# Kernel tuning notes

Measured on AMD Instinct MI355X. Metric: run time of the kernel, lower is better.

## Reference

```python
import jax, jax.numpy as jnp
import numpy as np


def setup_inputs() -> dict:
    key = jax.random.key(0)
    k1, k2 = jax.random.split(key)
    x1 = jax.random.normal(k1, (8192, 64), dtype=jnp.float32)
    x2 = jax.random.normal(k2, (8192, 64), dtype=jnp.float32)
    return {"x1": x1, "x2": x2}


def reference(x1, x2):
    # squared Euclidean distance: ||a-b||^2 = ||a||^2 + ||b||^2 - 2 a.b
    sq1 = jnp.sum(x1 * x1, axis=-1, keepdims=True)        # [N, 1]
    sq2 = jnp.sum(x2 * x2, axis=-1, keepdims=True).T      # [1, M]
    cross = jnp.einsum('nd,md->nm', x1, x2)               # [N, M] GEMM
    d2 = sq1 + sq2 - 2.0 * cross
    # clamp tiny negatives from floating-point cancellation (cdist>=0)
    return jnp.maximum(d2, 0.0)
```

## Files before the change

### kernel.cpp

```cpp
#include <hip/hip_runtime.h>


typedef __bf16 bf16x8 __attribute__((ext_vector_type(8)));
typedef float floatx4 __attribute__((ext_vector_type(4)));
typedef unsigned short ushort8 __attribute__((ext_vector_type(8)));

#define TILE 128
#define KD 64
#define LDSS 72

__device__ __forceinline__ unsigned short f2bf(float x) {
    union { float f; unsigned int u; } v; v.f = x;
    return (unsigned short)((v.u + 0x7FFFu + ((v.u >> 16) & 1u)) >> 16);
}

__global__ __launch_bounds__(256) void convert_rows(
        const float* __restrict__ x1,
        const float* __restrict__ x2,
        unsigned short* __restrict__ xb1,
        unsigned short* __restrict__ xb2,
        float* __restrict__ sq1,
        float* __restrict__ sq2,
        int N, int M) {
    const int tid = blockIdx.x * blockDim.x + threadIdx.x;
    if (tid >= N + M) return;
    const int r = (tid < N) ? tid : tid - N;
    const float* src = (tid < N) ? (x1 + (size_t)r * KD) : (x2 + (size_t)r * KD);
    unsigned short* dst = (tid < N) ? (xb1 + (size_t)r * KD) : (xb2 + (size_t)r * KD);
    float nrm = 0.f;
    #pragma unroll
    for (int i = 0; i < 8; ++i) {
        const float4 f0 = ((const float4*)src)[2 * i];
        const float4 f1 = ((const float4*)src)[2 * i + 1];
        nrm = fmaf(f0.x, f0.x, nrm); nrm = fmaf(f0.y, f0.y, nrm);
        nrm = fmaf(f0.z, f0.z, nrm); nrm = fmaf(f0.w, f0.w, nrm);
        nrm = fmaf(f1.x, f1.x, nrm); nrm = fmaf(f1.y, f1.y, nrm);
        nrm = fmaf(f1.z, f1.z, nrm); nrm = fmaf(f1.w, f1.w, nrm);
        ushort8 pk;
        pk[0] = f2bf(f0.x); pk[1] = f2bf(f0.y); pk[2] = f2bf(f0.z); pk[3] = f2bf(f0.w);
        pk[4] = f2bf(f1.x); pk[5] = f2bf(f1.y); pk[6] = f2bf(f1.z); pk[7] = f2bf(f1.w);
        *(ushort8*)&dst[i * 8] = pk;
    }
    if (tid < N) sq1[r] = nrm; else sq2[r] = nrm;
}

__global__ __launch_bounds__(256) void sqeuclid_main(
        const unsigned short* __restrict__ xb1,
        const unsigned short* __restrict__ xb2,
        const float* __restrict__ sq1,
        const float* __restrict__ sq2,
        float* __restrict__ out, int M) {
    const int t = threadIdx.x;
    const int block_row = blockIdx.y * TILE;
    const int block_col = blockIdx.x * TILE;
    const int wave = t >> 6, lane = t & 63;
    const int wr = (wave >> 1) * 64;
    const int wc = (wave & 1) * 64;
    const int lm = lane & 15, lq = lane >> 4;

    const int arow = block_row + wr + lm;
    const int brow = block_col + wc + lm;

    floatx4 acc[4][4];
    #pragma unroll
    for (int i = 0; i < 4; ++i)
        #pragma unroll
        for (int j = 0; j < 4; ++j)
            acc[i][j] = (floatx4){0.f, 0.f, 0.f, 0.f};

    #pragma unroll
    for (int ks = 0; ks < 2; ++ks) {
        const int koff = ks * 32 + lq * 8;
        bf16x8 afr[4], bfr[4];
        #pragma unroll
        for (int i = 0; i < 4; ++i) {
            afr[i] = *(const bf16x8*)&xb1[(size_t)(arow + i * 16) * KD + koff];
            bfr[i] = *(const bf16x8*)&xb2[(size_t)(brow + i * 16) * KD + koff];
        }
        #pragma unroll
        for (int i = 0; i < 4; ++i)
            #pragma unroll
            for (int j = 0; j < 4; ++j)
                acc[i][j] = __builtin_amdgcn_mfma_f32_16x16x32_bf16(
                    bfr[i], afr[j], acc[i][j], 0, 0, 0);
    }

    floatx4 s2q[4];
    #pragma unroll
    for (int i = 0; i < 4; ++i)
        s2q[i] = *(const floatx4*)&sq2[block_col + wc + i * 16 + lq * 4];

    #pragma unroll
    for (int j = 0; j < 4; ++j) {
        const int lrow = wr + j * 16 + lm;
        const float s1 = sq1[block_row + lrow];
        const size_t gbase = (size_t)(block_row + lrow) * M + block_col;
        #pragma unroll
        for (int i = 0; i < 4; ++i) {
            floatx4 v;
            #pragma unroll
            for (int r = 0; r < 4; ++r)
                v[r] = fmaxf(fmaf(-2.f, acc[i][j][r], s1 + s2q[i][r]), 0.f);
            *(floatx4*)(out + gbase + wc + i * 16 + lq * 4) = v;
        }
    }
}

__global__ void sqeuclid_fused(const float* __restrict__ x1,
                               const float* __restrict__ x2,
                               float* __restrict__ out, int M) {
    __shared__ unsigned short a_s[TILE][LDSS];
    __shared__ unsigned short b_s[TILE][LDSS];
    __shared__ float sq1_s[TILE];
    __shared__ float sq2_s[TILE];

    const int t = threadIdx.x;
    const int block_row = blockIdx.y * TILE;
    const int block_col = blockIdx.x * TILE;
    {
        const int r = t & 127;
        const float* src = (t < TILE) ? (x1 + (size_t)(block_row + r) * KD)
                                      : (x2 + (size_t)(block_col + r) * KD);
        unsigned short* dst = (t < TILE) ? a_s[r] : b_s[r];
        float nrm = 0.f;
        #pragma unroll
        for (int i = 0; i < 8; ++i) {
            const float4 f0 = ((const float4*)src)[2 * i];
            const float4 f1 = ((const float4*)src)[2 * i + 1];
            nrm = fmaf(f0.x, f0.x, nrm); nrm = fmaf(f0.y, f0.y, nrm);
            nrm = fmaf(f0.z, f0.z, nrm); nrm = fmaf(f0.w, f0.w, nrm);
            nrm = fmaf(f1.x, f1.x, nrm); nrm = fmaf(f1.y, f1.y, nrm);
            nrm = fmaf(f1.z, f1.z, nrm); nrm = fmaf(f1.w, f1.w, nrm);
            ushort8 pk;
            pk[0] = f2bf(f0.x); pk[1] = f2bf(f0.y); pk[2] = f2bf(f0.z); pk[3] = f2bf(f0.w);
            pk[4] = f2bf(f1.x); pk[5] = f2bf(f1.y); pk[6] = f2bf(f1.z); pk[7] = f2bf(f1.w);
            *(ushort8*)&dst[i * 8] = pk;
        }
        if (t < TILE) sq1_s[r] = nrm; else sq2_s[r] = nrm;
    }
    __syncthreads();

    const int wave = t >> 6, lane = t & 63;
    const int wr = (wave >> 1) * 64;
    const int wc = (wave & 1) * 64;
    const int lm = lane & 15, lq = lane >> 4;

    floatx4 acc[4][4];
    #pragma unroll
    for (int i = 0; i < 4; ++i)
        #pragma unroll
        for (int j = 0; j < 4; ++j)
            acc[i][j] = (floatx4){0.f, 0.f, 0.f, 0.f};

    #pragma unroll
    for (int ks = 0; ks < 2; ++ks) {
        const int koff = ks * 32 + lq * 8;
        bf16x8 afr[4], bfr[4];
        #pragma unroll
        for (int i = 0; i < 4; ++i) {
            afr[i] = *(const bf16x8*)&a_s[wr + i * 16 + lm][koff];
            bfr[i] = *(const bf16x8*)&b_s[wc + i * 16 + lm][koff];
        }
        #pragma unroll
        for (int i = 0; i < 4; ++i)
            #pragma unroll
            for (int j = 0; j < 4; ++j)
                acc[i][j] = __builtin_amdgcn_mfma_f32_16x16x32_bf16(
                    bfr[i], afr[j], acc[i][j], 0, 0, 0);
    }

    floatx4 s2q[4];
    #pragma unroll
    for (int i = 0; i < 4; ++i)
        s2q[i] = *(const floatx4*)&sq2_s[wc + i * 16 + lq * 4];

    #pragma unroll
    for (int j = 0; j < 4; ++j) {
        const int lrow = wr + j * 16 + lm;
        const float s1 = sq1_s[lrow];
        const size_t gbase = (size_t)(block_row + lrow) * M + block_col;
        #pragma unroll
        for (int i = 0; i < 4; ++i) {
            floatx4 v;
            #pragma unroll
            for (int r = 0; r < 4; ++r)
                v[r] = fmaxf(fmaf(-2.f, acc[i][j][r], s1 + s2q[i][r]), 0.f);
            *(floatx4*)(out + gbase + wc + i * 16 + lq * 4) = v;
        }
    }
}

extern "C" void kernel_launch(void* const* d_in, const int* in_sizes, int n_in,
                              void* d_out, int out_size, void* d_ws, size_t ws_size,
                              hipStream_t stream) {
    const float* x1 = (const float*)d_in[0];
    const float* x2 = (const float*)d_in[1];
    float* out = (float*)d_out;
    const int N = in_sizes[0] / KD;
    const int M = in_sizes[1] / KD;

    dim3 grid(M / TILE, N / TILE);
    dim3 block(256);

    const size_t xb1_off = 0;
    const size_t xb2_off = (size_t)N * KD * 2;
    const size_t sq1_off = xb2_off + (size_t)M * KD * 2;
    const size_t sq2_off = sq1_off + (size_t)N * 4;
    const size_t ws_needed = sq2_off + (size_t)M * 4;

    if (d_ws != nullptr && ws_size >= ws_needed) {
        unsigned short* xb1 = (unsigned short*)((char*)d_ws + xb1_off);
        unsigned short* xb2 = (unsigned short*)((char*)d_ws + xb2_off);
        float* sq1 = (float*)((char*)d_ws + sq1_off);
        float* sq2 = (float*)((char*)d_ws + sq2_off);
        const int rows = N + M;
        convert_rows<<<dim3((rows + 255) / 256), dim3(256), 0, stream>>>(
            x1, x2, xb1, xb2, sq1, sq2, N, M);
        sqeuclid_main<<<grid, block, 0, stream>>>(xb1, xb2, sq1, sq2, out, M);
    } else {
        sqeuclid_fused<<<grid, block, 0, stream>>>(x1, x2, out, M);
    }
}
```

Measured before the change: 274.4 us.

## Stage output tile through swizzled LDS for coalesced full-row stores with 64x256 tiles

```diff
diff --git a/kernel.cpp b/kernel.cpp
--- a/kernel.cpp
+++ b/kernel.cpp
@@ -5,8 +5,9 @@
 typedef float floatx4 __attribute__((ext_vector_type(4)));
 typedef unsigned short ushort8 __attribute__((ext_vector_type(8)));
 
-#define TILE 128
 #define KD 64
+#define TM 64
+#define TN 256
 #define LDSS 72
 
 __device__ __forceinline__ unsigned short f2bf(float x) {
@@ -50,16 +51,13 @@
         const float* __restrict__ sq1,
         const float* __restrict__ sq2,
         float* __restrict__ out, int M) {
+    __shared__ float out_s[TM * TN];
+
     const int t = threadIdx.x;
-    const int block_row = blockIdx.y * TILE;
-    const int block_col = blockIdx.x * TILE;
-    const int wave = t >> 6, lane = t & 63;
-    const int wr = (wave >> 1) * 64;
-    const int wc = (wave & 1) * 64;
+    const int block_row = blockIdx.y * TM;
+    const int block_col = blockIdx.x * TN;
+    const int w = t >> 6, lane = t & 63;
     const int lm = lane & 15, lq = lane >> 4;
-
-    const int arow = block_row + wr + lm;
-    const int brow = block_col + wc + lm;
 
     floatx4 acc[4][4];
     #pragma unroll
@@ -73,10 +71,11 @@
         const int koff = ks * 32 + lq * 8;
         bf16x8 afr[4], bfr[4];
         #pragma unroll
-        for (int i = 0; i < 4; ++i) {
-            afr[i] = *(const bf16x8*)&xb1[(size_t)(arow + i * 16) * KD + koff];
-            bfr[i] = *(const bf16x8*)&xb2[(size_t)(brow + i * 16) * KD + koff];
-        }
+        for (int j = 0; j < 4; ++j)
+            afr[j] = *(const bf16x8*)&xb1[(size_t)(block_row + j * 16 + lm) * KD + koff];
+        #pragma unroll
+        for (int i = 0; i < 4; ++i)
+            bfr[i] = *(const bf16x8*)&xb2[(size_t)(block_col + w * 64 + i * 16 + lm) * KD + koff];
         #pragma unroll
         for (int i = 0; i < 4; ++i)
             #pragma unroll
@@ -88,40 +87,50 @@
     floatx4 s2q[4];
     #pragma unroll
     for (int i = 0; i < 4; ++i)
-        s2q[i] = *(const floatx4*)&sq2[block_col + wc + i * 16 + lq * 4];
+        s2q[i] = *(const floatx4*)&sq2[block_col + w * 64 + i * 16 + lq * 4];
 
     #pragma unroll
     for (int j = 0; j < 4; ++j) {
-        const int lrow = wr + j * 16 + lm;
-        const float s1 = sq1[block_row + lrow];
-        const size_t gbase = (size_t)(block_row + lrow) * M + block_col;
+        const int row = j * 16 + lm;
+        const float s1 = sq1[block_row + row];
         #pragma unroll
         for (int i = 0; i < 4; ++i) {
+            const int qi = w * 16 + i * 4 + lq;
+            const int qi_sw = qi ^ lm;
             floatx4 v;
             #pragma unroll
             for (int r = 0; r < 4; ++r)
                 v[r] = fmaxf(fmaf(-2.f, acc[i][j][r], s1 + s2q[i][r]), 0.f);
-            *(floatx4*)(out + gbase + wc + i * 16 + lq * 4) = v;
-        }
+            *(floatx4*)&out_s[row * TN + qi_sw * 4] = v;
+        }
+    }
+    __syncthreads();
+
+    #pragma unroll
+    for (int k = 0; k < 16; ++k) {
+        const int row = k * 4 + w;
+        const int qi_sw = lane ^ (row & 15);
+        const floatx4 v = *(const floatx4*)&out_s[row * TN + qi_sw * 4];
+        *(floatx4*)(out + (size_t)(block_row + row) * M + block_col + lane * 4) = v;
     }
 }
 
 __global__ void sqeuclid_fused(const float* __restrict__ x1,
                                const float* __restrict__ x2,
                                float* __restrict__ out, int M) {
-    __shared__ unsigned short a_s[TILE][LDSS];
-    __shared__ unsigned short b_s[TILE][LDSS];
-    __shared__ float sq1_s[TILE];
-    __shared__ float sq2_s[TILE];
+    __shared__ unsigned short a_s[128][LDSS];
+    __shared__ unsigned short b_s[128][LDSS];
+    __shared__ float sq1_s[128];
+    __shared__ float sq2_s[128];
 
     const int t = threadIdx.x;
-    const int block_row = blockIdx.y * TILE;
-    const int block_col = blockIdx.x * TILE;
+    const int block_row = blockIdx.y * 128;
+    const int block_col = blockIdx.x * 128;
     {
         const int r = t & 127;
-        const float* src = (t < TILE) ? (x1 + (size_t)(block_row + r) * KD)
-                                      : (x2 + (size_t)(block_col + r) * KD);
-        unsigned short* dst = (t < TILE) ? a_s[r] : b_s[r];
+        const float* src = (t < 128) ? (x1 + (size_t)(block_row + r) * KD)
+                                     : (x2 + (size_t)(block_col + r) * KD);
+        unsigned short* dst = (t < 128) ? a_s[r] : b_s[r];
         float nrm = 0.f;
         #pragma unroll
         for (int i = 0; i < 8; ++i) {
@@ -136,7 +145,7 @@
             pk[4] = f2bf(f1.x); pk[5] = f2bf(f1.y); pk[6] = f2bf(f1.z); pk[7] = f2bf(f1.w);
             *(ushort8*)&dst[i * 8] = pk;
         }
-        if (t < TILE) sq1_s[r] = nrm; else sq2_s[r] = nrm;
+        if (t < 128) sq1_s[r] = nrm; else sq2_s[r] = nrm;
     }
     __syncthreads();
 
@@ -199,9 +208,6 @@
     const int N = in_sizes[0] / KD;
     const int M = in_sizes[1] / KD;
 
-    dim3 grid(M / TILE, N / TILE);
-    dim3 block(256);
-
     const size_t xb1_off = 0;
     const size_t xb2_off = (size_t)N * KD * 2;
     const size_t sq1_off = xb2_off + (size_t)M * KD * 2;
@@ -216,8 +222,10 @@
         const int rows = N + M;
         convert_rows<<<dim3((rows + 255) / 256), dim3(256), 0, stream>>>(
             x1, x2, xb1, xb2, sq1, sq2, N, M);
-        sqeuclid_main<<<grid, block, 0, stream>>>(xb1, xb2, sq1, sq2, out, M);
+        dim3 grid(M / TN, N / TM);
+        sqeuclid_main<<<grid, dim3(256), 0, stream>>>(xb1, xb2, sq1, sq2, out, M);
     } else {
-        sqeuclid_fused<<<grid, block, 0, stream>>>(x1, x2, out, M);
-    }
-}
+        dim3 grid(M / 128, N / 128);
+        sqeuclid_fused<<<grid, dim3(256), 0, stream>>>(x1, x2, out, M);
+    }
+}
```

New measurement: 282.8 us. 1.03x slower.
